# Optimization experiments

Hardware: AMD Instinct MI355X
Metric: run time of the kernel (lower is better)

## Reference

```python
import jax, jax.numpy as jnp
import numpy as np

K = 16  # FLAGS.num_neighbors
N = 2562  # ellipsoid vertices
B = 4     # FLAGS.batch_size
M = 16384 # points per cloud
D = 3     # coordinate dim


def _mean_neighborhood(coord, pc, k):
    # coord: [N, D] query vertices; pc: [B, D, M] point cloud (channels-first)
    x2 = jnp.sum(coord * coord, axis=1)[None, :, None]          # [1, N, 1]
    y2 = jnp.sum(pc * pc, axis=1)[:, None, :]                   # [B, 1, M]
    xy = jnp.einsum('nd,bdm->bnm', coord, pc)                   # [B, N, M]
    d2 = x2 + y2 - 2.0 * xy                                     # [B, N, M]
    _, idx = jax.lax.top_k(-d2, k)                               # [B, N, K] indices into M
    Y = jnp.transpose(pc, (0, 2, 1))                             # [B, M, D]
    bv = jnp.arange(pc.shape[0])[:, None, None]                  # [B, 1, 1]
    knnY = Y[bv, idx]                                            # [B, N, K, D]
    knnY_mean = jnp.mean(knnY, axis=2)                           # [B, N, D]
    return knnY_mean[0]                                          # [N, D] (matches knnY_mean[0])


def setup_inputs() -> dict:
    key = jax.random.key(0)
    ks = jax.random.split(key, 5)
    inputs = jax.random.normal(ks[0], (N, D), dtype=jnp.float32)
    pcs = [jax.random.normal(ks[i + 1], (B, D, M), dtype=jnp.float32) for i in range(4)]
    return {"inputs": inputs, "pc0": pcs[0], "pc1": pcs[1], "pc2": pcs[2], "pc3": pcs[3]}


def reference(inputs, pc0, pc1, pc2, pc3):
    s0 = _mean_neighborhood(inputs, pc0, K)
    s1 = _mean_neighborhood(inputs, pc1, K)
    s2 = _mean_neighborhood(inputs, pc2, K)
    s3 = _mean_neighborhood(inputs, pc3, K)
    return jnp.concatenate([inputs, s0, s1, s2, s3], axis=1)  # [N, 5*D]
```

## Files before the change

kernel.cpp:

```cpp
#include <hip/hip_runtime.h>
#include <stdint.h>
#include <math.h>

#define NQ    2562
#define MPTS  16384
#define QPB   2
#define NBQ   1281
#define NT    (MPTS / 256)
#define CAP   320

__global__ __launch_bounds__(256)
void passthrough_kernel(const float* __restrict__ inp, float* __restrict__ out) {
    int gid = blockIdx.x * 256 + threadIdx.x;
    if (gid < NQ * 3) {
        int n = gid / 3, c = gid - n * 3;
        out[n * 15 + c] = inp[gid];
    }
}

__device__ __forceinline__ float sqsum3(float y0, float y1, float y2) {
    return __fadd_rn(__fadd_rn(__fmul_rn(y0, y0), __fmul_rn(y1, y1)),
                     __fmul_rn(y2, y2));
}
__device__ __forceinline__ float keyf(float xs, float a2, float b2, float c2,
                                      float y0, float y1, float y2, float ysq) {
    float u = fmaf(c2, y2, fmaf(b2, y1, __fmul_rn(a2, y0)));
    return __fsub_rn(__fadd_rn(xs, ysq), u);
}
__device__ __forceinline__ unsigned long long packkey(float k, int m) {
    uint32_t kb = __float_as_uint(k);
    kb ^= (uint32_t)((int32_t)kb >> 31) | 0x80000000u;
    return ((unsigned long long)kb << 32) | (unsigned)m;
}
__device__ __forceinline__ float unmapkey(unsigned long long pk) {
    uint32_t kb = (uint32_t)(pk >> 32);
    return __uint_as_float((kb & 0x80000000u) ? (kb ^ 0x80000000u) : ~kb);
}
__device__ __forceinline__ int prefix_lt(unsigned long long m) {
    return __builtin_amdgcn_mbcnt_hi((unsigned)(m >> 32),
           __builtin_amdgcn_mbcnt_lo((unsigned)m, 0u));
}

__device__ __forceinline__ unsigned long long sort64(unsigned long long v, int lane) {
#pragma unroll
    for (int k = 2; k <= 64; k <<= 1) {
#pragma unroll
        for (int j = k >> 1; j > 0; j >>= 1) {
            unsigned long long p = __shfl_xor(v, j);
            bool up = ((lane & k) == 0) == ((lane & j) == 0);
            bool sw = up ? (p < v) : (v < p);
            v = sw ? p : v;
        }
    }
    return v;
}

__device__ __forceinline__ float rebuild_q(unsigned long long* t16p,
                                           unsigned long long* S, int& cnt,
                                           int lane, bool fin) {
    int c = cnt;
    int full = c >> 6, rem = c & 63;
    int rounds = full + ((fin && rem) ? 1 : 0);
    unsigned long long v = ~0ULL;
    for (int rd = 0; rd < rounds; ++rd) {
        int i = (rd << 6) + lane;
        unsigned long long pk = (i < c) ? S[i] : ~0ULL;
        pk = sort64(pk, lane);
        unsigned long long bsw = __shfl(pk, (31 - lane) & 63);
        v = (lane < 16) ? t16p[lane & 15] : (lane < 32) ? bsw : ~0ULL;
#pragma unroll
        for (int j = 16; j > 0; j >>= 1) {
            unsigned long long p2 = __shfl_xor(v, j);
            bool keepmin = (lane & j) == 0;
            bool less = p2 < v;
            v = (keepmin == less) ? p2 : v;
        }
        if (lane < 16) t16p[lane] = v;
    }
    if (!fin) {
        if (lane < rem) S[lane] = S[(full << 6) + lane];
        cnt = rem;
    } else {
        cnt = 0;
    }
    return unmapkey(__shfl(v, 15));
}

__global__ __launch_bounds__(256)
void ysq_kernel(const float* __restrict__ pc0, const float* __restrict__ pc1,
                const float* __restrict__ pc2, const float* __restrict__ pc3,
                float* __restrict__ ysq) {
    int gid = blockIdx.x * 256 + threadIdx.x;
    int pc = gid >> 14, m = gid & (MPTS - 1);
    const float* P = (pc == 0) ? pc0 : (pc == 1) ? pc1 : (pc == 2) ? pc2 : pc3;
    ysq[gid] = sqsum3(P[m], P[MPTS + m], P[2 * MPTS + m]);
}

template <bool USE_YSQ>
__global__ __launch_bounds__(128)
void knn_kernel(const float* __restrict__ inp,
                const float* __restrict__ pc0, const float* __restrict__ pc1,
                const float* __restrict__ pc2, const float* __restrict__ pc3,
                const float* __restrict__ ysq,
                float* __restrict__ out) {
    const int b    = blockIdx.x;
    const int wid  = threadIdx.x >> 6;
    const int lane = threadIdx.x & 63;

    const int pc = b / NBQ;
    const int nb = b - pc * NBQ;
    const float* __restrict__ P = (pc == 0) ? pc0 : (pc == 1) ? pc1
                                : (pc == 2) ? pc2 : pc3;

    __shared__ unsigned long long stk_sh[2][CAP];
    __shared__ unsigned long long t16_sh[2][16];

    if (lane < 16) t16_sh[wid][lane] = ~0ULL;

    float A2, B2, C2, XS;
    const int n = QPB * nb + wid;
    {
        float x0 = inp[n * 3 + 0];
        float x1 = inp[n * 3 + 1];
        float x2 = inp[n * 3 + 2];
        A2 = 2.0f * x0;
        B2 = 2.0f * x1;
        C2 = 2.0f * x2;
        XS = sqsum3(x0, x1, x2);
    }
    float tau;
    int   cnt = 0;

    const float* __restrict__ Pl = P + (lane << 2);
    const float* __restrict__ Ql = ysq + pc * MPTS + (lane << 2);

    auto push_tile = [&](int mofs, float k0, float k1, float k2, float k3) {
        unsigned long long b0 = __ballot(k0 <= tau);
        unsigned long long b1 = __ballot(k1 <= tau);
        unsigned long long b2 = __ballot(k2 <= tau);
        unsigned long long b3 = __ballot(k3 <= tau);
        int pre = prefix_lt(b0) + prefix_lt(b1) + prefix_lt(b2) + prefix_lt(b3);
        int tot = __popcll(b0) + __popcll(b1) + __popcll(b2) + __popcll(b3);
        int pos = cnt + pre;
        unsigned long long* S = stk_sh[wid];
        if (k0 <= tau) S[pos++] = packkey(k0, mofs + 0);
        if (k1 <= tau) S[pos++] = packkey(k1, mofs + 1);
        if (k2 <= tau) S[pos++] = packkey(k2, mofs + 2);
        if (k3 <= tau) S[pos++] = packkey(k3, mofs + 3);
        cnt += tot;
        if (cnt >= 64)
            tau = rebuild_q(t16_sh[wid], S, cnt, lane, false);
    };

    {
        float4 ax = *(const float4*)(Pl);
        float4 ay = *(const float4*)(Pl + MPTS);
        float4 az = *(const float4*)(Pl + 2 * MPTS);
        float q0, q1, q2, q3;
        if (USE_YSQ) {
            float4 aq = *(const float4*)(Ql);
            q0 = aq.x; q1 = aq.y; q2 = aq.z; q3 = aq.w;
        } else {
            q0 = sqsum3(ax.x, ay.x, az.x);
            q1 = sqsum3(ax.y, ay.y, az.y);
            q2 = sqsum3(ax.z, ay.z, az.z);
            q3 = sqsum3(ax.w, ay.w, az.w);
        }
        float k0 = keyf(XS, A2, B2, C2, ax.x, ay.x, az.x, q0);
        float k1 = keyf(XS, A2, B2, C2, ax.y, ay.y, az.y, q1);
        float k2 = keyf(XS, A2, B2, C2, ax.z, ay.z, az.z, q2);
        float k3 = keyf(XS, A2, B2, C2, ax.w, ay.w, az.w, q3);
        float km = fminf(fminf(k0, k1), fminf(k2, k3));
        float g = km;
        g = fminf(g, __shfl_xor(g, 1));
        g = fminf(g, __shfl_xor(g, 2));
        float m = g;
        m = fmaxf(m, __shfl_xor(m, 4));
        m = fmaxf(m, __shfl_xor(m, 8));
        m = fmaxf(m, __shfl_xor(m, 16));
        m = fmaxf(m, __shfl_xor(m, 32));
        tau = m;
        push_tile(lane << 2, k0, k1, k2, k3);
    }

    float4 cx = *(const float4*)(Pl + 256);
    float4 cy = *(const float4*)(Pl + MPTS + 256);
    float4 cz = *(const float4*)(Pl + 2 * MPTS + 256);
    float4 cq;
    if (USE_YSQ) cq = *(const float4*)(Ql + 256);

    for (int t = 1; t < NT; ++t) {
        const int tn = (t + 1 < NT) ? t + 1 : t;
        float4 nx = *(const float4*)(Pl + (tn << 8));
        float4 ny = *(const float4*)(Pl + MPTS + (tn << 8));
        float4 nz = *(const float4*)(Pl + 2 * MPTS + (tn << 8));
        float4 nq;
        if (USE_YSQ) nq = *(const float4*)(Ql + (tn << 8));

        const int mofs = (t << 8) + (lane << 2);
        float q0, q1, q2, q3;
        if (USE_YSQ) {
            q0 = cq.x; q1 = cq.y; q2 = cq.z; q3 = cq.w;
        } else {
            q0 = sqsum3(cx.x, cy.x, cz.x);
            q1 = sqsum3(cx.y, cy.y, cz.y);
            q2 = sqsum3(cx.z, cy.z, cz.z);
            q3 = sqsum3(cx.w, cy.w, cz.w);
        }
        float k0 = keyf(XS, A2, B2, C2, cx.x, cy.x, cz.x, q0);
        float k1 = keyf(XS, A2, B2, C2, cx.y, cy.y, cz.y, q1);
        float k2 = keyf(XS, A2, B2, C2, cx.z, cy.z, cz.z, q2);
        float k3 = keyf(XS, A2, B2, C2, cx.w, cy.w, cz.w, q3);
        float km = fminf(fminf(k0, k1), fminf(k2, k3));
        if (__ballot(km <= tau))
            push_tile(mofs, k0, k1, k2, k3);

        cx = nx; cy = ny; cz = nz;
        if (USE_YSQ) cq = nq;
    }

    if (cnt > 0)
        rebuild_q(t16_sh[wid], stk_sh[wid], cnt, lane, true);

    if (lane < 16) {
        unsigned long long v = t16_sh[wid][lane];
        int idx = (int)(unsigned)v;
        float gx = P[idx];
        float gy = P[MPTS + idx];
        float gz = P[2 * MPTS + idx];
#pragma unroll
        for (int off = 8; off > 0; off >>= 1) {
            gx += __shfl_down(gx, off, 16);
            gy += __shfl_down(gy, off, 16);
            gz += __shfl_down(gz, off, 16);
        }
        if (lane == 0) {
            float* o = out + n * 15 + 3 + 3 * pc;
            o[0] = gx * 0.0625f;
            o[1] = gy * 0.0625f;
            o[2] = gz * 0.0625f;
        }
    }
}

extern "C" void kernel_launch(void* const* d_in, const int* in_sizes, int n_in,
                              void* d_out, int out_size, void* d_ws, size_t ws_size,
                              hipStream_t stream) {
    const float* inp = (const float*)d_in[0];
    const float* pc0 = (const float*)d_in[1];
    const float* pc1 = (const float*)d_in[2];
    const float* pc2 = (const float*)d_in[3];
    const float* pc3 = (const float*)d_in[4];
    float* out = (float*)d_out;
    float* ysq = (float*)d_ws;

    hipLaunchKernelGGL(passthrough_kernel, dim3((NQ * 3 + 255) / 256), dim3(256),
                       0, stream, inp, out);

    const bool use_ysq = (ws_size >= (size_t)(4 * MPTS * sizeof(float)));
    if (use_ysq) {
        hipLaunchKernelGGL(ysq_kernel, dim3(4 * MPTS / 256), dim3(256), 0, stream,
                           pc0, pc1, pc2, pc3, ysq);
        hipLaunchKernelGGL((knn_kernel<true>), dim3(4 * NBQ), dim3(128), 0, stream,
                           inp, pc0, pc1, pc2, pc3, ysq, out);
    } else {
        hipLaunchKernelGGL((knn_kernel<false>), dim3(4 * NBQ), dim3(128), 0, stream,
                           inp, pc0, pc1, pc2, pc3, ysq, out);
    }
}
```

Baseline: 104.3 us.

## Store candidate indices only in LDS stack and recompute keys during rebuild

```diff
diff --git a/kernel.cpp b/kernel.cpp
--- a/kernel.cpp
+++ b/kernel.cpp
@@ -56,15 +56,20 @@
 }
 
 __device__ __forceinline__ float rebuild_q(unsigned long long* t16p,
-                                           unsigned long long* S, int& cnt,
-                                           int lane, bool fin) {
+                                           unsigned* S, int& cnt, int lane,
+                                           const float* __restrict__ P,
+                                           float xs, float a2, float b2, float c2,
+                                           bool fin) {
     int c = cnt;
     int full = c >> 6, rem = c & 63;
     int rounds = full + ((fin && rem) ? 1 : 0);
     unsigned long long v = ~0ULL;
     for (int rd = 0; rd < rounds; ++rd) {
         int i = (rd << 6) + lane;
-        unsigned long long pk = (i < c) ? S[i] : ~0ULL;
+        unsigned idx = (i < c) ? S[i] : 0u;
+        float y0 = P[idx], y1 = P[MPTS + idx], y2 = P[2 * MPTS + idx];
+        float key = keyf(xs, a2, b2, c2, y0, y1, y2, sqsum3(y0, y1, y2));
+        unsigned long long pk = (i < c) ? packkey(key, (int)idx) : ~0ULL;
         pk = sort64(pk, lane);
         unsigned long long bsw = __shfl(pk, (31 - lane) & 63);
         v = (lane < 16) ? t16p[lane & 15] : (lane < 32) ? bsw : ~0ULL;
@@ -112,7 +117,7 @@
     const float* __restrict__ P = (pc == 0) ? pc0 : (pc == 1) ? pc1
                                 : (pc == 2) ? pc2 : pc3;
 
-    __shared__ unsigned long long stk_sh[2][CAP];
+    __shared__ unsigned           stk_sh[2][CAP];
     __shared__ unsigned long long t16_sh[2][16];
 
     if (lane < 16) t16_sh[wid][lane] = ~0ULL;
@@ -142,14 +147,14 @@
         int pre = prefix_lt(b0) + prefix_lt(b1) + prefix_lt(b2) + prefix_lt(b3);
         int tot = __popcll(b0) + __popcll(b1) + __popcll(b2) + __popcll(b3);
         int pos = cnt + pre;
-        unsigned long long* S = stk_sh[wid];
-        if (k0 <= tau) S[pos++] = packkey(k0, mofs + 0);
-        if (k1 <= tau) S[pos++] = packkey(k1, mofs + 1);
-        if (k2 <= tau) S[pos++] = packkey(k2, mofs + 2);
-        if (k3 <= tau) S[pos++] = packkey(k3, mofs + 3);
+        unsigned* S = stk_sh[wid];
+        if (k0 <= tau) S[pos++] = (unsigned)(mofs + 0);
+        if (k1 <= tau) S[pos++] = (unsigned)(mofs + 1);
+        if (k2 <= tau) S[pos++] = (unsigned)(mofs + 2);
+        if (k3 <= tau) S[pos++] = (unsigned)(mofs + 3);
         cnt += tot;
         if (cnt >= 64)
-            tau = rebuild_q(t16_sh[wid], S, cnt, lane, false);
+            tau = rebuild_q(t16_sh[wid], S, cnt, lane, P, XS, A2, B2, C2, false);
     };
 
     {
@@ -183,44 +188,33 @@
         push_tile(lane << 2, k0, k1, k2, k3);
     }
 
-    float4 cx = *(const float4*)(Pl + 256);
-    float4 cy = *(const float4*)(Pl + MPTS + 256);
-    float4 cz = *(const float4*)(Pl + 2 * MPTS + 256);
-    float4 cq;
-    if (USE_YSQ) cq = *(const float4*)(Ql + 256);
-
+#pragma unroll 2
     for (int t = 1; t < NT; ++t) {
-        const int tn = (t + 1 < NT) ? t + 1 : t;
-        float4 nx = *(const float4*)(Pl + (tn << 8));
-        float4 ny = *(const float4*)(Pl + MPTS + (tn << 8));
-        float4 nz = *(const float4*)(Pl + 2 * MPTS + (tn << 8));
-        float4 nq;
-        if (USE_YSQ) nq = *(const float4*)(Ql + (tn << 8));
-
         const int mofs = (t << 8) + (lane << 2);
+        float4 xv = *(const float4*)(Pl + (t << 8));
+        float4 yv = *(const float4*)(Pl + MPTS + (t << 8));
+        float4 zv = *(const float4*)(Pl + 2 * MPTS + (t << 8));
         float q0, q1, q2, q3;
         if (USE_YSQ) {
-            q0 = cq.x; q1 = cq.y; q2 = cq.z; q3 = cq.w;
+            float4 qv = *(const float4*)(Ql + (t << 8));
+            q0 = qv.x; q1 = qv.y; q2 = qv.z; q3 = qv.w;
         } else {
-            q0 = sqsum3(cx.x, cy.x, cz.x);
-            q1 = sqsum3(cx.y, cy.y, cz.y);
-            q2 = sqsum3(cx.z, cy.z, cz.z);
-            q3 = sqsum3(cx.w, cy.w, cz.w);
-        }
-        float k0 = keyf(XS, A2, B2, C2, cx.x, cy.x, cz.x, q0);
-        float k1 = keyf(XS, A2, B2, C2, cx.y, cy.y, cz.y, q1);
-        float k2 = keyf(XS, A2, B2, C2, cx.z, cy.z, cz.z, q2);
-        float k3 = keyf(XS, A2, B2, C2, cx.w, cy.w, cz.w, q3);
+            q0 = sqsum3(xv.x, yv.x, zv.x);
+            q1 = sqsum3(xv.y, yv.y, zv.y);
+            q2 = sqsum3(xv.z, yv.z, zv.z);
+            q3 = sqsum3(xv.w, yv.w, zv.w);
+        }
+        float k0 = keyf(XS, A2, B2, C2, xv.x, yv.x, zv.x, q0);
+        float k1 = keyf(XS, A2, B2, C2, xv.y, yv.y, zv.y, q1);
+        float k2 = keyf(XS, A2, B2, C2, xv.z, yv.z, zv.z, q2);
+        float k3 = keyf(XS, A2, B2, C2, xv.w, yv.w, zv.w, q3);
         float km = fminf(fminf(k0, k1), fminf(k2, k3));
         if (__ballot(km <= tau))
             push_tile(mofs, k0, k1, k2, k3);
-
-        cx = nx; cy = ny; cz = nz;
-        if (USE_YSQ) cq = nq;
     }
 
     if (cnt > 0)
-        rebuild_q(t16_sh[wid], stk_sh[wid], cnt, lane, true);
+        rebuild_q(t16_sh[wid], stk_sh[wid], cnt, lane, P, XS, A2, B2, C2, true);
 
     if (lane < 16) {
         unsigned long long v = t16_sh[wid][lane];
```

After: 113.1 us. +8.5%, slower.
